# Optimization experiments

Hardware: AMD Instinct MI355X
Metric: run time of the kernel (lower is better)

Reference implementation:

```python
import jax, jax.numpy as jnp
import numpy as np

B_SZ, L, H, P = 8, 8192, 1024, 64  # batch, seq, d_inner, ssm_size
CONJ_SYM = True
DT_MIN, DT_MAX, DT_FLOOR = 1e-3, 1e-1, 1e-4


def setup_inputs() -> dict:
    key = jax.random.key(0)
    ks = jax.random.split(key, 8)
    u = jax.random.normal(ks[0], (B_SZ, L, H), dtype=jnp.float32)
    h_real = jnp.zeros((B_SZ, P), dtype=jnp.float32)
    h_imag = jnp.zeros((B_SZ, P), dtype=jnp.float32)
    # HiPPO-like stable init: Re(Lambda) = -0.5, Im(Lambda) = pi*k
    A_real = -0.5 * jnp.ones((P,), dtype=jnp.float32)
    A_imag = jnp.pi * jnp.arange(P, dtype=jnp.float32)
    local_P = 2 * P if CONJ_SYM else P
    b_scale = np.sqrt(1.0 / local_P).astype(np.float32)
    c_scale = np.sqrt(1.0 / H).astype(np.float32)
    B_real = jax.random.normal(ks[1], (P, H), dtype=jnp.float32) * b_scale
    B_imag = jax.random.normal(ks[2], (P, H), dtype=jnp.float32) * b_scale
    C_real = jax.random.normal(ks[3], (H, P), dtype=jnp.float32) * c_scale
    C_imag = jax.random.normal(ks[4], (H, P), dtype=jnp.float32) * c_scale
    D = jax.random.normal(ks[5], (H,), dtype=jnp.float32)
    # torch init: dt = exp(U(log dt_min, log dt_max)).clamp(dt_floor); inv_dt = dt + log(-expm1(-dt))
    log_dt = jax.random.uniform(ks[6], (P,), dtype=jnp.float32) \
        * (np.log(DT_MAX) - np.log(DT_MIN)) + np.log(DT_MIN)
    dt0 = jnp.clip(jnp.exp(log_dt), DT_FLOOR, None)
    inv_dt = dt0 + jnp.log(-jnp.expm1(-dt0))
    return {"u": u, "h_real": h_real, "h_imag": h_imag,
            "A_real": A_real, "A_imag": A_imag,
            "B_real": B_real, "B_imag": B_imag,
            "C_real": C_real, "C_imag": C_imag,
            "D": D, "inv_dt": inv_dt}


def reference(u, h_real, h_imag, A_real, A_imag, B_real, B_imag,
              C_real, C_imag, D, inv_dt):
    A = A_real + 1j * A_imag            # (P,)
    Bm = B_real + 1j * B_imag           # (P, H)
    Cm = C_real + 1j * C_imag           # (H, P)
    dt = jax.nn.softplus(inv_dt)        # step_rescale = 1.0
    # bilinear discretization
    den = 1.0 - (dt / 2.0) * A
    dA = (1.0 + (dt / 2.0) * A) / den   # (P,)
    dB = (dt / den)[:, None] * Bm       # (P, H)
    # input projection: Bu[b,l,p] = sum_h dB[p,h] * u[b,l,h]
    Bu = jnp.einsum('blh,ph->blp', u, dB)              # complex64 (B, L, P)
    h0 = h_real + 1j * h_imag                          # (B, P)
    Bu = Bu.at[:, 0].add(dA * h0)                      # fold initial state in
    a = jnp.broadcast_to(dA, Bu.shape)
    def combine(e1, e2):
        a1, b1 = e1
        a2, b2 = e2
        return a2 * a1, a2 * b1 + b2
    _, hs = jax.lax.associative_scan(combine, (a, Bu), axis=1)  # (B, L, P)
    yc = jnp.einsum('blp,hp->blh', hs, Cm)
    scale = 2.0 if CONJ_SYM else 1.0
    y = scale * yc.real + D * u
    h_last = hs[:, -1]
    return y, h_last.real, h_last.imag
```

## Files before the change

### kernel.cpp

```cpp
#include <hip/hip_runtime.h>

typedef unsigned short ushort_t;
typedef short s8v __attribute__((ext_vector_type(8)));
typedef unsigned short ushort8 __attribute__((ext_vector_type(8)));
typedef float floatx4 __attribute__((ext_vector_type(4)));

#define MFMA16(a, b, c) __builtin_amdgcn_mfma_f32_16x16x32_bf16((a), (b), (c), 0, 0, 0)

static constexpr int B_SZ = 8;
static constexpr int L = 8192;
static constexpr int H = 1024;
static constexpr int P = 64;
static constexpr int M_TOT = B_SZ * L;
static constexpr int S_CH = 64;
static constexpr int NC = L / S_CH;

__device__ inline ushort_t f2bf(float f) {
    union { float f; unsigned u; } v; v.f = f;
    unsigned r = v.u + 0x7fffu + ((v.u >> 16) & 1u);
    return (ushort_t)(r >> 16);
}

__global__ void params_kernel(const float* __restrict__ A_real,
                              const float* __restrict__ A_imag,
                              const float* __restrict__ inv_dt,
                              float* __restrict__ params,
                              float* __restrict__ dApow) {
    int p = threadIdx.x;
    float x = inv_dt[p];
    float dt = (x > 20.f) ? x : log1pf(expf(x));
    float ar = A_real[p], ai = A_imag[p];
    float dr = 1.f - 0.5f * dt * ar;
    float di = -0.5f * dt * ai;
    float inv = 1.f / fmaf(dr, dr, di * di);
    float nr = 1.f + 0.5f * dt * ar, ni = 0.5f * dt * ai;
    float dAr = (nr * dr + ni * di) * inv;
    float dAi = (ni * dr - nr * di) * inv;
    params[p]       = dAr;
    params[64 + p]  = dAi;
    params[128 + p] = dt * dr * inv;
    params[192 + p] = -dt * di * inv;
    float pr = 1.f, pi = 0.f;
    dApow[2 * p] = 1.f; dApow[2 * p + 1] = 0.f;
    for (int k = 1; k <= S_CH; k++) {
        float npr = pr * dAr - pi * dAi;
        float npi = pr * dAi + pi * dAr;
        pr = npr; pi = npi;
        dApow[k * 128 + 2 * p]     = pr;
        dApow[k * 128 + 2 * p + 1] = pi;
    }
}

__global__ void build_w(const float* __restrict__ Br, const float* __restrict__ Bi,
                        const float* __restrict__ Cr, const float* __restrict__ Ci,
                        const float* __restrict__ params,
                        ushort_t* __restrict__ W1T, ushort_t* __restrict__ CeffT) {
    int t = blockIdx.x * 256 + threadIdx.x;
    if (t < 128 * 1024) {
        int n = t >> 10, k = t & 1023;
        int p = n >> 1;
        float sr = params[128 + p], si = params[192 + p];
        float br = Br[p * 1024 + k], bi = Bi[p * 1024 + k];
        float v = (n & 1) ? (sr * bi + si * br) : (sr * br - si * bi);
        W1T[t] = f2bf(v);
    } else {
        int t2 = t - 128 * 1024;
        int h = t2 >> 7, k = t2 & 127;
        int p = k >> 1;
        float v = (k & 1) ? -2.f * Ci[h * 64 + p] : 2.f * Cr[h * 64 + p];
        CeffT[t2] = f2bf(v);
    }
}

__global__ __launch_bounds__(256) void gemm1(const float* __restrict__ u,
                                             const ushort_t* __restrict__ W1T,
                                             float* __restrict__ Bu) {
    __shared__ ushort_t As[128][40];
    __shared__ ushort_t Bs[128][40];
    int tid = threadIdx.x;
    int wave = tid >> 6, lane = tid & 63;
    int q = lane >> 4, mn = lane & 15;
    size_t row0 = (size_t)blockIdx.x * 128;
    int r = tid >> 1, half = tid & 1;

    floatx4 acc[2][8] = {};

    for (int kk = 0; kk < 1024; kk += 32) {
        __syncthreads();
        {
            const float4* up = (const float4*)(u + (row0 + r) * 1024 + kk + half * 16);
            float4 f0 = up[0], f1 = up[1], f2 = up[2], f3 = up[3];
            ushort8 t0, t1;
            t0[0] = f2bf(f0.x); t0[1] = f2bf(f0.y); t0[2] = f2bf(f0.z); t0[3] = f2bf(f0.w);
            t0[4] = f2bf(f1.x); t0[5] = f2bf(f1.y); t0[6] = f2bf(f1.z); t0[7] = f2bf(f1.w);
            t1[0] = f2bf(f2.x); t1[1] = f2bf(f2.y); t1[2] = f2bf(f2.z); t1[3] = f2bf(f2.w);
            t1[4] = f2bf(f3.x); t1[5] = f2bf(f3.y); t1[6] = f2bf(f3.z); t1[7] = f2bf(f3.w);
            ushort8* dst = (ushort8*)&As[r][half * 16];
            dst[0] = t0; dst[1] = t1;
            const ushort8* wp = (const ushort8*)(W1T + r * 1024 + kk + half * 16);
            ushort8* db = (ushort8*)&Bs[r][half * 16];
            db[0] = wp[0]; db[1] = wp[1];
        }
        __syncthreads();
        s8v a0 = *(const s8v*)&As[wave * 32 + mn][q * 8];
        s8v a1 = *(const s8v*)&As[wave * 32 + 16 + mn][q * 8];
        #pragma unroll
        for (int j = 0; j < 8; j++) {
            s8v bf = *(const s8v*)&Bs[j * 16 + mn][q * 8];
            acc[0][j] = MFMA16(a0, bf, acc[0][j]);
            acc[1][j] = MFMA16(a1, bf, acc[1][j]);
        }
    }
    #pragma unroll
    for (int i = 0; i < 2; i++)
        #pragma unroll
        for (int j = 0; j < 8; j++)
            #pragma unroll
            for (int reg = 0; reg < 4; reg++) {
                size_t row = row0 + wave * 32 + i * 16 + q * 4 + reg;
                Bu[row * 128 + j * 16 + mn] = acc[i][j][reg];
            }
}

__global__ __launch_bounds__(256) void scan_local(float* __restrict__ Bu,
                                                  const float* __restrict__ params,
                                                  float* __restrict__ endbuf) {
    int tid = threadIdx.x;
    int p = tid & 63;
    int chunk = blockIdx.x * 4 + (tid >> 6);
    int b = chunk >> 7, c = chunk & (NC - 1);
    float dAr = params[p], dAi = params[64 + p];
    float* base = Bu + ((size_t)b * L + (size_t)c * S_CH) * 128 + 2 * p;
    float hr = 0.f, hi = 0.f;
    float2 cur = *(const float2*)base;
    float2 nxt;
    #pragma unroll 4
    for (int l = 0; l < S_CH; l++) {
        if (l < S_CH - 1) nxt = *(const float2*)(base + (size_t)(l + 1) * 128);
        float nhr = fmaf(dAr, hr, fmaf(-dAi, hi, cur.x));
        float nhi = fmaf(dAr, hi, fmaf(dAi, hr, cur.y));
        hr = nhr; hi = nhi;
        *(float2*)(base + (size_t)l * 128) = make_float2(hr, hi);
        cur = nxt;
    }
    float* e = endbuf + (size_t)chunk * 128 + 2 * p;
    e[0] = hr; e[1] = hi;
}

__global__ void scan_carry(const float* __restrict__ endbuf,
                           const float* __restrict__ dApow,
                           const float* __restrict__ h0r,
                           const float* __restrict__ h0i,
                           float* __restrict__ carry) {
    int t = blockIdx.x * 64 + threadIdx.x;
    int b = t >> 6, p = t & 63;
    float aSr = dApow[S_CH * 128 + 2 * p], aSi = dApow[S_CH * 128 + 2 * p + 1];
    float cr = h0r[b * 64 + p], ci = h0i[b * 64 + p];
    for (int c = 0; c < NC; c++) {
        float* dst = carry + ((size_t)b * NC + c) * 128 + 2 * p;
        dst[0] = cr; dst[1] = ci;
        const float* e = endbuf + ((size_t)b * NC + c) * 128 + 2 * p;
        float er = e[0], ei = e[1];
        float nr = fmaf(aSr, cr, fmaf(-aSi, ci, er));
        float ni = fmaf(aSr, ci, fmaf(aSi, cr, ei));
        cr = nr; ci = ni;
    }
}

__global__ __launch_bounds__(256) void gemm2(const float* __restrict__ hloc,
                                             const ushort_t* __restrict__ CeffT,
                                             const float* __restrict__ u,
                                             const float* __restrict__ D,
                                             const float* __restrict__ dApow,
                                             const float* __restrict__ carry,
                                             float* __restrict__ y,
                                             float* __restrict__ out_hlast) {
    __shared__ ushort_t As[128][136];
    __shared__ ushort_t Bs[128][136];
    int tid = threadIdx.x;
    int wave = tid >> 6, lane = tid & 63;
    int q = lane >> 4, mn = lane & 15;
    size_t row0 = (size_t)blockIdx.x * 128;
    int r = tid >> 1, half = tid & 1;
    {
        size_t rrow = row0 + r;
        int b = (int)(rrow >> 13);
        int l = (int)(rrow & (L - 1));
        int c = l >> 6;
        int kp = (l & (S_CH - 1)) + 1;
        const float4* hp = (const float4*)(hloc + rrow * 128 + half * 64);
        const float4* pw = (const float4*)(dApow + (size_t)kp * 128 + half * 64);
        const float4* cv = (const float4*)(carry + ((size_t)b * NC + c) * 128 + half * 64);
        ushort8* dst = (ushort8*)&As[r][half * 64];
        bool last = (l == L - 1);
        #pragma unroll
        for (int j = 0; j < 8; j++) {
            float4 hv0 = hp[2 * j], hv1 = hp[2 * j + 1];
            float4 p0 = pw[2 * j], p1 = pw[2 * j + 1];
            float4 c0 = cv[2 * j], c1 = cv[2 * j + 1];
            float r0 = hv0.x + p0.x * c0.x - p0.y * c0.y;
            float i0 = hv0.y + p0.x * c0.y + p0.y * c0.x;
            float r1 = hv0.z + p0.z * c0.z - p0.w * c0.w;
            float i1 = hv0.w + p0.z * c0.w + p0.w * c0.z;
            float r2 = hv1.x + p1.x * c1.x - p1.y * c1.y;
            float i2 = hv1.y + p1.x * c1.y + p1.y * c1.x;
            float r3 = hv1.z + p1.z * c1.z - p1.w * c1.w;
            float i3 = hv1.w + p1.z * c1.w + p1.w * c1.z;
            ushort8 o;
            o[0] = f2bf(r0); o[1] = f2bf(i0); o[2] = f2bf(r1); o[3] = f2bf(i1);
            o[4] = f2bf(r2); o[5] = f2bf(i2); o[6] = f2bf(r3); o[7] = f2bf(i3);
            dst[j] = o;
            if (last) {
                int pb = (half * 64 + j * 8) >> 1;
                out_hlast[b * 64 + pb]           = r0; out_hlast[512 + b * 64 + pb]     = i0;
                out_hlast[b * 64 + pb + 1]       = r1; out_hlast[512 + b * 64 + pb + 1] = i1;
                out_hlast[b * 64 + pb + 2]       = r2; out_hlast[512 + b * 64 + pb + 2] = i2;
                out_hlast[b * 64 + pb + 3]       = r3; out_hlast[512 + b * 64 + pb + 3] = i3;
            }
        }
    }
    for (int ct = 0; ct < 8; ct++) {
        __syncthreads();
        {
            const ushort8* src = (const ushort8*)(CeffT + (size_t)(ct * 128 + r) * 128 + half * 64);
            ushort8* dst = (ushort8*)&Bs[r][half * 64];
            #pragma unroll
            for (int i = 0; i < 8; i++) dst[i] = src[i];
        }
        __syncthreads();
        floatx4 acc[2][8] = {};
        #pragma unroll
        for (int kk = 0; kk < 128; kk += 32) {
            s8v a0 = *(const s8v*)&As[wave * 32 + mn][kk + q * 8];
            s8v a1 = *(const s8v*)&As[wave * 32 + 16 + mn][kk + q * 8];
            #pragma unroll
            for (int j = 0; j < 8; j++) {
                s8v bf = *(const s8v*)&Bs[j * 16 + mn][kk + q * 8];
                acc[0][j] = MFMA16(a0, bf, acc[0][j]);
                acc[1][j] = MFMA16(a1, bf, acc[1][j]);
            }
        }
        float dv[8];
        #pragma unroll
        for (int j = 0; j < 8; j++) dv[j] = D[ct * 128 + j * 16 + mn];
        #pragma unroll
        for (int i = 0; i < 2; i++)
            #pragma unroll
            for (int j = 0; j < 8; j++) {
                int col = ct * 128 + j * 16 + mn;
                #pragma unroll
                for (int reg = 0; reg < 4; reg++) {
                    size_t row = row0 + wave * 32 + i * 16 + q * 4 + reg;
                    y[row * 1024 + col] = acc[i][j][reg] + dv[j] * u[row * 1024 + col];
                }
            }
    }
}

extern "C" void kernel_launch(void* const* d_in, const int* in_sizes, int n_in,
                              void* d_out, int out_size, void* d_ws, size_t ws_size,
                              hipStream_t stream) {
    const float* u      = (const float*)d_in[0];
    const float* h_r    = (const float*)d_in[1];
    const float* h_i    = (const float*)d_in[2];
    const float* A_real = (const float*)d_in[3];
    const float* A_imag = (const float*)d_in[4];
    const float* B_real = (const float*)d_in[5];
    const float* B_imag = (const float*)d_in[6];
    const float* C_real = (const float*)d_in[7];
    const float* C_imag = (const float*)d_in[8];
    const float* D      = (const float*)d_in[9];
    const float* inv_dt = (const float*)d_in[10];
    float* out = (float*)d_out;

    float* wsf       = (float*)d_ws;
    float* P_params  = wsf;
    float* P_dApow   = wsf + 1024;
    float* P_carry   = wsf + 1024 + 8448;
    float* P_end     = P_carry + 131072;
    ushort_t* P_W1T  = (ushort_t*)(P_end + 131072);
    ushort_t* P_Ceff = P_W1T + 128 * 1024;
    float* P_Bu      = (float*)(P_Ceff + 1024 * 128);

    params_kernel<<<1, 64, 0, stream>>>(A_real, A_imag, inv_dt, P_params, P_dApow);
    build_w<<<1024, 256, 0, stream>>>(B_real, B_imag, C_real, C_imag, P_params, P_W1T, P_Ceff);
    gemm1<<<M_TOT / 128, 256, 0, stream>>>(u, P_W1T, P_Bu);
    scan_local<<<B_SZ * NC / 4, 256, 0, stream>>>(P_Bu, P_params, P_end);
    scan_carry<<<8, 64, 0, stream>>>(P_end, P_dApow, h_r, h_i, P_carry);
    gemm2<<<M_TOT / 128, 256, 0, stream>>>(P_Bu, P_Ceff, u, D, P_dApow, P_carry,
                                           out, out + (size_t)M_TOT * H);
}
```

Before: 605.8 us.

## Fuse chunk-local scan into input-projection GEMM epilogue using shared memory

The intra-chunk linear recurrence is folded into the first GEMM: each block writes its 128x128 Bu tile into LDS, each wave scans 32 rows, and the waves are then stitched together with powers of dA, so only the chunk-local states are written to global memory. This removes the separate scan_local kernel and its extra read-modify-write pass over the Bu buffer. The chunk size doubles to 128, which halves the sequential carry-scan length. In exchange the block uses 64KB of LDS, which may lower occupancy, and the per-wave serial scan plus carry loop adds latency to the GEMM epilogue.

```diff
diff --git a/kernel.cpp b/kernel.cpp
--- a/kernel.cpp
+++ b/kernel.cpp
@@ -10,9 +10,8 @@
 static constexpr int B_SZ = 8;
 static constexpr int L = 8192;
 static constexpr int H = 1024;
-static constexpr int P = 64;
 static constexpr int M_TOT = B_SZ * L;
-static constexpr int S_CH = 64;
+static constexpr int S_CH = 128;
 static constexpr int NC = L / S_CH;
 
 __device__ inline ushort_t f2bf(float f) {
@@ -72,11 +71,15 @@
     }
 }
 
-__global__ __launch_bounds__(256) void gemm1(const float* __restrict__ u,
-                                             const ushort_t* __restrict__ W1T,
-                                             float* __restrict__ Bu) {
-    __shared__ ushort_t As[128][40];
-    __shared__ ushort_t Bs[128][40];
+__global__ __launch_bounds__(256) void gemm1s(const float* __restrict__ u,
+                                              const ushort_t* __restrict__ W1T,
+                                              const float* __restrict__ params,
+                                              const float* __restrict__ dApow,
+                                              float* __restrict__ hloc,
+                                              float* __restrict__ endbuf) {
+    __shared__ float bus[128 * 128];
+    ushort_t* As = (ushort_t*)bus;
+    ushort_t* Bs = As + 128 * 40;
     int tid = threadIdx.x;
     int wave = tid >> 6, lane = tid & 63;
     int q = lane >> 4, mn = lane & 15;
@@ -95,56 +98,72 @@
             t0[4] = f2bf(f1.x); t0[5] = f2bf(f1.y); t0[6] = f2bf(f1.z); t0[7] = f2bf(f1.w);
             t1[0] = f2bf(f2.x); t1[1] = f2bf(f2.y); t1[2] = f2bf(f2.z); t1[3] = f2bf(f2.w);
             t1[4] = f2bf(f3.x); t1[5] = f2bf(f3.y); t1[6] = f2bf(f3.z); t1[7] = f2bf(f3.w);
-            ushort8* dst = (ushort8*)&As[r][half * 16];
+            ushort8* dst = (ushort8*)&As[r * 40 + half * 16];
             dst[0] = t0; dst[1] = t1;
             const ushort8* wp = (const ushort8*)(W1T + r * 1024 + kk + half * 16);
-            ushort8* db = (ushort8*)&Bs[r][half * 16];
+            ushort8* db = (ushort8*)&Bs[r * 40 + half * 16];
             db[0] = wp[0]; db[1] = wp[1];
         }
         __syncthreads();
-        s8v a0 = *(const s8v*)&As[wave * 32 + mn][q * 8];
-        s8v a1 = *(const s8v*)&As[wave * 32 + 16 + mn][q * 8];
+        s8v a0 = *(const s8v*)&As[(wave * 32 + mn) * 40 + q * 8];
+        s8v a1 = *(const s8v*)&As[(wave * 32 + 16 + mn) * 40 + q * 8];
         #pragma unroll
         for (int j = 0; j < 8; j++) {
-            s8v bf = *(const s8v*)&Bs[j * 16 + mn][q * 8];
+            s8v bf = *(const s8v*)&Bs[(j * 16 + mn) * 40 + q * 8];
             acc[0][j] = MFMA16(a0, bf, acc[0][j]);
             acc[1][j] = MFMA16(a1, bf, acc[1][j]);
         }
     }
+    __syncthreads();
     #pragma unroll
     for (int i = 0; i < 2; i++)
         #pragma unroll
         for (int j = 0; j < 8; j++)
             #pragma unroll
             for (int reg = 0; reg < 4; reg++) {
-                size_t row = row0 + wave * 32 + i * 16 + q * 4 + reg;
-                Bu[row * 128 + j * 16 + mn] = acc[i][j][reg];
+                int row = wave * 32 + i * 16 + q * 4 + reg;
+                bus[row * 128 + j * 16 + mn] = acc[i][j][reg];
             }
-}
-
-__global__ __launch_bounds__(256) void scan_local(float* __restrict__ Bu,
-                                                  const float* __restrict__ params,
-                                                  float* __restrict__ endbuf) {
-    int tid = threadIdx.x;
-    int p = tid & 63;
-    int chunk = blockIdx.x * 4 + (tid >> 6);
-    int b = chunk >> 7, c = chunk & (NC - 1);
-    float dAr = params[p], dAi = params[64 + p];
-    float* base = Bu + ((size_t)b * L + (size_t)c * S_CH) * 128 + 2 * p;
+    __syncthreads();
+
+    float dAr = params[lane], dAi = params[64 + lane];
     float hr = 0.f, hi = 0.f;
-    float2 cur = *(const float2*)base;
-    float2 nxt;
+    int base = wave * 32 * 128 + 2 * lane;
     #pragma unroll 4
-    for (int l = 0; l < S_CH; l++) {
-        if (l < S_CH - 1) nxt = *(const float2*)(base + (size_t)(l + 1) * 128);
-        float nhr = fmaf(dAr, hr, fmaf(-dAi, hi, cur.x));
-        float nhi = fmaf(dAr, hi, fmaf(dAi, hr, cur.y));
+    for (int t = 0; t < 32; t++) {
+        float2 v = *(float2*)&bus[base + t * 128];
+        float nhr = fmaf(dAr, hr, fmaf(-dAi, hi, v.x));
+        float nhi = fmaf(dAr, hi, fmaf(dAi, hr, v.y));
         hr = nhr; hi = nhi;
-        *(float2*)(base + (size_t)l * 128) = make_float2(hr, hi);
-        cur = nxt;
-    }
-    float* e = endbuf + (size_t)chunk * 128 + 2 * p;
-    e[0] = hr; e[1] = hi;
+        *(float2*)&bus[base + t * 128] = make_float2(hr, hi);
+    }
+    __syncthreads();
+
+    float a32r = dApow[32 * 128 + 2 * lane], a32i = dApow[32 * 128 + 2 * lane + 1];
+    float cr = 0.f, ci = 0.f;
+    for (int w2 = 0; w2 < wave; w2++) {
+        float2 e = *(float2*)&bus[(w2 * 32 + 31) * 128 + 2 * lane];
+        float tr = fmaf(a32r, cr, fmaf(-a32i, ci, e.x));
+        float ti = fmaf(a32r, ci, fmaf(a32i, cr, e.y));
+        cr = tr; ci = ti;
+    }
+
+    float* gbase = hloc + (row0 + wave * 32) * 128 + 2 * lane;
+    float lr = 0.f, li = 0.f;
+    #pragma unroll 4
+    for (int t = 0; t < 32; t++) {
+        float2 v = *(float2*)&bus[base + t * 128];
+        float pr = dApow[(t + 1) * 128 + 2 * lane];
+        float pi = dApow[(t + 1) * 128 + 2 * lane + 1];
+        float orr = v.x + pr * cr - pi * ci;
+        float oi  = v.y + pr * ci + pi * cr;
+        *(float2*)(gbase + (size_t)t * 128) = make_float2(orr, oi);
+        lr = orr; li = oi;
+    }
+    if (wave == 3) {
+        float* e = endbuf + (size_t)blockIdx.x * 128 + 2 * lane;
+        e[0] = lr; e[1] = li;
+    }
 }
 
 __global__ void scan_carry(const float* __restrict__ endbuf,
@@ -186,7 +205,7 @@
         size_t rrow = row0 + r;
         int b = (int)(rrow >> 13);
         int l = (int)(rrow & (L - 1));
-        int c = l >> 6;
+        int c = l >> 7;
         int kp = (l & (S_CH - 1)) + 1;
         const float4* hp = (const float4*)(hloc + rrow * 128 + half * 64);
         const float4* pw = (const float4*)(dApow + (size_t)kp * 128 + half * 64);
@@ -276,16 +295,15 @@
     float* wsf       = (float*)d_ws;
     float* P_params  = wsf;
     float* P_dApow   = wsf + 1024;
-    float* P_carry   = wsf + 1024 + 8448;
-    float* P_end     = P_carry + 131072;
-    ushort_t* P_W1T  = (ushort_t*)(P_end + 131072);
+    float* P_carry   = wsf + 1024 + 16640;
+    float* P_end     = P_carry + 65536;
+    ushort_t* P_W1T  = (ushort_t*)(P_end + 65536);
     ushort_t* P_Ceff = P_W1T + 128 * 1024;
     float* P_Bu      = (float*)(P_Ceff + 1024 * 128);
 
     params_kernel<<<1, 64, 0, stream>>>(A_real, A_imag, inv_dt, P_params, P_dApow);
     build_w<<<1024, 256, 0, stream>>>(B_real, B_imag, C_real, C_imag, P_params, P_W1T, P_Ceff);
-    gemm1<<<M_TOT / 128, 256, 0, stream>>>(u, P_W1T, P_Bu);
-    scan_local<<<B_SZ * NC / 4, 256, 0, stream>>>(P_Bu, P_params, P_end);
+    gemm1s<<<M_TOT / 128, 256, 0, stream>>>(u, P_W1T, P_params, P_dApow, P_Bu, P_end);
     scan_carry<<<8, 64, 0, stream>>>(P_end, P_dApow, h_r, h_i, P_carry);
     gemm2<<<M_TOT / 128, 256, 0, stream>>>(P_Bu, P_Ceff, u, D, P_dApow, P_carry,
                                            out, out + (size_t)M_TOT * H);
```

Result: faster. 592.2 us (-2.3%).
